# Performance work log

Hardware: AMD Instinct MI355X
Metric: run time of the kernel (lower is better)

## Reference

```python
import jax, jax.numpy as jnp
import numpy as np

B, S, D, H = 2, 2048, 1024, 16
DH = D // H  # 64


def setup_inputs() -> dict:
    key = jax.random.key(0)
    ks = jax.random.split(key, 9)
    def rn(k, shape, scale=1.0):
        return jax.random.normal(k, shape, dtype=jnp.float32) * scale
    w_scale = 1.0 / np.sqrt(D)
    return {
        "queries": rn(ks[0], (B, S, D)),
        "keys": rn(ks[1], (B, S, D)),
        "values": rn(ks[2], (B, S, D)),
        "Wq": rn(ks[3], (D, D), w_scale),
        "bq": rn(ks[4], (D,), w_scale),
        "Wk": rn(ks[5], (D, D), w_scale),
        "bk": rn(ks[6], (D,), w_scale),
        "Wv": rn(ks[7], (D, D), w_scale),
        "bv": rn(ks[8], (D,), w_scale),
    }


def _split_heads(x):
    # torch: cat(split(x, DH, dim=-1), dim=0) -> index (h*B + b); equivalent to
    # [B,S,H,DH] -> [H,B,S,DH]
    bsz, slen, _ = x.shape
    return x.reshape(bsz, slen, H, DH).transpose(2, 0, 1, 3)


def reference(queries, keys, values, Wq, bq, Wk, bk, Wv, bv):
    # Linear projections (W stored so that y = x @ W + b)
    Q = queries @ Wq + bq
    K = keys @ Wk + bk
    V = values @ Wv + bv

    Qh = _split_heads(Q)  # [H,B,S,DH]
    Kh = _split_heads(K)
    Vh = _split_heads(V)

    scale = 1.0 / jnp.sqrt(jnp.asarray(DH, dtype=Qh.dtype))
    scores = jnp.einsum("hbqd,hbkd->hbqk", Qh, Kh) * scale  # [H,B,S,S]
    attn = jax.nn.softmax(scores, axis=-1)  # dropout_rate=0 -> identity
    out = jnp.einsum("hbqk,hbkd->hbqd", attn, Vh)  # [H,B,S,DH]

    # torch: cat(split(out, B, dim=0), dim=2) -> [B,S,H*DH] with head h in slice h
    out = out.transpose(1, 2, 0, 3).reshape(queries.shape[0], queries.shape[1], D)
    return out + queries  # residual; NOTE: W_O is defined but unused in the original forward
```

## Files before the change

kernel.cpp:

```cpp
#include <hip/hip_runtime.h>
#include <hip/hip_bf16.h>
#include <math.h>

#define BB 2
#define SS 2048
#define DD 1024
#define HH 16
#define DHH 64
#define MM (BB * SS)

typedef float f32x4 __attribute__((ext_vector_type(4)));
typedef float f32x16 __attribute__((ext_vector_type(16)));
typedef __bf16 bf16x8 __attribute__((ext_vector_type(8)));
typedef unsigned int u32x2 __attribute__((ext_vector_type(2)));

#define N_QKV ((size_t)MM * DD)
#define N_W   ((size_t)DD * DD)

__device__ unsigned short g_X [3][N_QKV];
__device__ unsigned short g_Q [N_QKV];
__device__ unsigned short g_K [N_QKV];
__device__ unsigned short g_Vt[N_QKV];
__device__ unsigned short g_Wt[3][N_W];

__device__ __forceinline__ unsigned short f2bu(float f) {
    unsigned u = __float_as_uint(f);
    unsigned r = u + 0x7FFFu + ((u >> 16) & 1u);
    return (unsigned short)(r >> 16);
}

union FragU { uint4 u; bf16x8 v; unsigned short s[8]; };
static __device__ __forceinline__ bf16x8 ldfrag(const unsigned short* p) {
    FragU f; f.u = *(const uint4*)p; return f.v;
}

static __device__ __forceinline__ unsigned pkbf(float a, float b) {
    union { __bf16 h[2]; unsigned u; } w;
    w.h[0] = (__bf16)a; w.h[1] = (__bf16)b;
    return w.u;
}

static __device__ __forceinline__ float fexp2(float x) {
#if __has_builtin(__builtin_amdgcn_exp2f)
    return __builtin_amdgcn_exp2f(x);
#else
    float r;
    asm("v_exp_f32 %0, %1" : "=v"(r) : "v"(x));
    return r;
#endif
}

static __device__ __forceinline__ void plswap(unsigned &a, unsigned &b) {
#if __has_builtin(__builtin_amdgcn_permlane32_swap)
    u32x2 r = __builtin_amdgcn_permlane32_swap((int)a, (int)b, false, false);
    a = r[0]; b = r[1];
#else
    asm volatile("v_permlane32_swap_b32 %0, %1" : "+v"(a), "+v"(b));
#endif
}

__global__ __launch_bounds__(256) void cvt3(
        const float* __restrict__ x0, const float* __restrict__ x1,
        const float* __restrict__ x2, unsigned short* __restrict__ X)
{
    const float* src = blockIdx.y == 0 ? x0 : (blockIdx.y == 1 ? x1 : x2);
    unsigned short* dst = X + (size_t)blockIdx.y * N_QKV;
    const size_t i = ((size_t)blockIdx.x * 256 + threadIdx.x) * 4;
    const float4 v = *(const float4*)(src + i);
    ushort4 s;
    s.x = f2bu(v.x); s.y = f2bu(v.y); s.z = f2bu(v.z); s.w = f2bu(v.w);
    *(ushort4*)(dst + i) = s;
}

__global__ __launch_bounds__(256) void transpose_w3(
        const float* __restrict__ W0, const float* __restrict__ W1,
        const float* __restrict__ W2, unsigned short* __restrict__ Wt3)
{
    const float* W = blockIdx.z == 0 ? W0 : (blockIdx.z == 1 ? W1 : W2);
    unsigned short* Wt = Wt3 + (size_t)blockIdx.z * N_W;
    __shared__ float Ts[64][65];
    const int t = threadIdx.x;
    const int k0 = blockIdx.y * 64, n0 = blockIdx.x * 64;
#pragma unroll
    for (int i = 0; i < 16; ++i) {
        const int f = t + 256 * i, r = f >> 6, c = f & 63;
        Ts[r][c] = W[(size_t)(k0 + r) * DD + n0 + c];
    }
    __syncthreads();
#pragma unroll
    for (int i = 0; i < 16; ++i) {
        const int f = t + 256 * i, r = f >> 6, c = f & 63;
        Wt[(size_t)(n0 + r) * DD + k0 + c] = f2bu(Ts[c][r]);
    }
}

__global__ __launch_bounds__(256) void proj3(
        const unsigned short* __restrict__ X, const unsigned short* __restrict__ Wt3,
        const float* __restrict__ bq, const float* __restrict__ bk,
        const float* __restrict__ bv,
        unsigned short* __restrict__ Qp, unsigned short* __restrict__ Kp,
        unsigned short* __restrict__ Vtp)
{
    const int z = blockIdx.z;
    const unsigned short* xb = X   + (size_t)z * N_QKV;
    const unsigned short* Wt = Wt3 + (size_t)z * N_W;
    const float* bias = z == 0 ? bq : (z == 1 ? bk : bv);
    const float scale = z == 0 ? 0.18033688011112042f : 1.0f;

    __shared__ unsigned short As[128][72];
    __shared__ unsigned short Bs[128][72];
    const int t = threadIdx.x, lane = t & 63, w = t >> 6;
    const int q = lane >> 4, li = lane & 15;
    const int wm = (w >> 1) * 64, wn = (w & 1) * 64;
    const int m0 = blockIdx.y * 128, n0 = blockIdx.x * 128;
    const int rs = t >> 3, cs = (t & 7) * 8;

    f32x4 acc[4][4];
#pragma unroll
    for (int mt = 0; mt < 4; ++mt)
#pragma unroll
        for (int nt = 0; nt < 4; ++nt) acc[mt][nt] = (f32x4)0.f;

    uint4 pa0, pa1, pa2, pa3, pb0, pb1, pb2, pb3;
#define PROJ_LD(kk) \
    pa0 = *(const uint4*)(xb + (size_t)(m0 + rs      ) * DD + (kk) + cs); \
    pa1 = *(const uint4*)(xb + (size_t)(m0 + rs + 32 ) * DD + (kk) + cs); \
    pa2 = *(const uint4*)(xb + (size_t)(m0 + rs + 64 ) * DD + (kk) + cs); \
    pa3 = *(const uint4*)(xb + (size_t)(m0 + rs + 96 ) * DD + (kk) + cs); \
    pb0 = *(const uint4*)(Wt + (size_t)(n0 + rs      ) * DD + (kk) + cs); \
    pb1 = *(const uint4*)(Wt + (size_t)(n0 + rs + 32 ) * DD + (kk) + cs); \
    pb2 = *(const uint4*)(Wt + (size_t)(n0 + rs + 64 ) * DD + (kk) + cs); \
    pb3 = *(const uint4*)(Wt + (size_t)(n0 + rs + 96 ) * DD + (kk) + cs);

    PROJ_LD(0)

    for (int kk = 0; kk < DD; kk += 64) {
        *(uint4*)&As[rs     ][cs] = pa0;
        *(uint4*)&As[rs + 32][cs] = pa1;
        *(uint4*)&As[rs + 64][cs] = pa2;
        *(uint4*)&As[rs + 96][cs] = pa3;
        *(uint4*)&Bs[rs     ][cs] = pb0;
        *(uint4*)&Bs[rs + 32][cs] = pb1;
        *(uint4*)&Bs[rs + 64][cs] = pb2;
        *(uint4*)&Bs[rs + 96][cs] = pb3;
        __syncthreads();
        if (kk + 64 < DD) { PROJ_LD(kk + 64) }
#pragma unroll
        for (int ks = 0; ks < 64; ks += 32) {
            bf16x8 a[4], b[4];
#pragma unroll
            for (int mt = 0; mt < 4; ++mt) a[mt] = ldfrag(&As[wm + mt * 16 + li][ks + q * 8]);
#pragma unroll
            for (int nt = 0; nt < 4; ++nt) b[nt] = ldfrag(&Bs[wn + nt * 16 + li][ks + q * 8]);
#pragma unroll
            for (int mt = 0; mt < 4; ++mt)
#pragma unroll
                for (int nt = 0; nt < 4; ++nt)
                    acc[mt][nt] = __builtin_amdgcn_mfma_f32_16x16x32_bf16(
                        a[mt], b[nt], acc[mt][nt], 0, 0, 0);
        }
        __syncthreads();
    }
#undef PROJ_LD

    float bvv[4];
#pragma unroll
    for (int nt = 0; nt < 4; ++nt) bvv[nt] = bias[n0 + wn + nt * 16 + li];

    if (z < 2) {
        unsigned short* out = z == 0 ? Qp : Kp;
#pragma unroll
        for (int mt = 0; mt < 4; ++mt)
#pragma unroll
            for (int nt = 0; nt < 4; ++nt)
#pragma unroll
                for (int reg = 0; reg < 4; ++reg) {
                    const int m = m0 + wm + mt * 16 + q * 4 + reg;
                    out[(size_t)m * DD + n0 + wn + nt * 16 + li] =
                        f2bu((acc[mt][nt][reg] + bvv[nt]) * scale);
                }
    } else {
        const int b = m0 >> 11;
        const int h = (n0 + wn) >> 6;
#pragma unroll
        for (int mt = 0; mt < 4; ++mt)
#pragma unroll
            for (int nt = 0; nt < 4; ++nt) {
                const int s = (m0 & (SS - 1)) + wm + mt * 16 + q * 4;
                const int dh = nt * 16 + li;
                ushort4 sv;
                sv.x = f2bu(acc[mt][nt][0] + bvv[nt]);
                sv.y = f2bu(acc[mt][nt][1] + bvv[nt]);
                sv.z = f2bu(acc[mt][nt][2] + bvv[nt]);
                sv.w = f2bu(acc[mt][nt][3] + bvv[nt]);
                *(ushort4*)(Vtp + ((size_t)((b * HH + h) * DHH + dh)) * SS + s) = sv;
            }
    }
}

__global__ __launch_bounds__(512, 2) void attn9(
        const unsigned short* __restrict__ Qg, const unsigned short* __restrict__ Kg,
        const unsigned short* __restrict__ Vtg,
        const float* __restrict__ queries, float* __restrict__ outp)
{
    __shared__ unsigned short KVb[2][2][2][64][64];
    __shared__ float Lp[2][4][32];

    const int t = threadIdx.x, lane = t & 63;
    const int g  = t >> 8;
    const int wg = (t >> 6) & 3;
    const int col = lane & 31;
    const int hi  = lane >> 5;

    const int bid = blockIdx.x;
    const int slot = bid >> 3;
    const int p = (bid & 7) + 8 * (slot >> 4);
    const int qt = slot & 15;
    const int h = p & 15;
    const int b = p >> 4;

    const int tg = t & 255;
    const int sr = tg >> 3;
    const int sc = tg & 7;

    unsigned short (*Kb)[64][64] = KVb[g][0];
    unsigned short (*Vb)[64][64] = KVb[g][1];

    const unsigned short* Kbase = Kg  + (size_t)(b * SS) * DD + h * DHH;
    const unsigned short* Vbase = Vtg + ((size_t)((b * HH + h) * DHH)) * SS;

    bf16x8 qa[4];
    {
        const unsigned short* qp =
            Qg + (size_t)(b * SS + qt * 128 + wg * 32 + col) * DD + h * DHH + hi * 8;
#pragma unroll
        for (int i = 0; i < 4; ++i) qa[i] = ldfrag(qp + i * 16);
    }

    f32x16 o0 = (f32x16)0.f, o1 = (f32x16)0.f;
    float lsum = 0.f;
    const int xr2 = (col ^ (col >> 3)) & 7;
    const int wsw = (sr ^ (sr >> 3)) & 7;
    const int kvofs = g << 10;

    uint4 aK0, aK1, aV0, aV1, bK0, bK1, bV0, bV1;
#define LD_SET(K0, K1, V0, V1, s0) \
    K0 = *(const uint4*)(Kbase + (size_t)((s0) + sr     ) * DD + sc * 8); \
    K1 = *(const uint4*)(Kbase + (size_t)((s0) + sr + 32) * DD + sc * 8); \
    V0 = *(const uint4*)(Vbase + (size_t)(sr     ) * SS + (s0) + sc * 8); \
    V1 = *(const uint4*)(Vbase + (size_t)(sr + 32) * SS + (s0) + sc * 8);

#define ST_SET(K0, K1, V0, V1, buf) \
    *(uint4*)&Kb[buf][sr     ][(sc ^ wsw) * 8]     = K0; \
    *(uint4*)&Kb[buf][sr + 32][(sc ^ wsw ^ 4) * 8] = K1; \
    *(uint4*)&Vb[buf][sr     ][(sc ^ wsw) * 8]     = V0; \
    *(uint4*)&Vb[buf][sr + 32][(sc ^ wsw ^ 4) * 8] = V1;

#define KT_BODY(CUR, LDG, STG, LDQ4, STQ4)                                    \
    {                                                                         \
        if (LDG) { LD_SET LDQ4 }                                              \
                       \
        f32x16 st0 = (f32x16)0.f, st1 = (f32x16)0.f;                          \
        __builtin_amdgcn_s_setprio(1);                                        \
        _Pragma("unroll")                                                     \
        for (int i = 0; i < 4; ++i) {                                         \
            const int sl = (i * 2 + hi) ^ xr2;                                \
            bf16x8 ka0 = ldfrag(&Kb[CUR][col     ][sl * 8]);                  \
            bf16x8 ka1 = ldfrag(&Kb[CUR][col + 32][(sl ^ 4) * 8]);            \
            st0 = __builtin_amdgcn_mfma_f32_32x32x16_bf16(ka0, qa[i], st0, 0, 0, 0); \
            st1 = __builtin_amdgcn_mfma_f32_32x32x16_bf16(ka1, qa[i], st1, 0, 0, 0); \
        }                                                                     \
        __builtin_amdgcn_s_setprio(0);                                        \
                                 \
        unsigned pkw[4][4];                                                   \
        float ls = 0.f;                                                       \
        _Pragma("unroll")                                                     \
        for (int s = 0; s < 2; ++s) {                                         \
            float pe[8];                                                      \
            _Pragma("unroll")                                                 \
            for (int r = 0; r < 8; ++r) pe[r] = fexp2(st0[8 * s + r]);        \
            ls += ((pe[0] + pe[1]) + (pe[2] + pe[3])) + ((pe[4] + pe[5]) + (pe[6] + pe[7])); \
            pkw[s][0] = pkbf(pe[0], pe[1]); pkw[s][1] = pkbf(pe[2], pe[3]);   \
            pkw[s][2] = pkbf(pe[4], pe[5]); pkw[s][3] = pkbf(pe[6], pe[7]);   \
        }                                                                     \
        _Pragma("unroll")                                                     \
        for (int s = 0; s < 2; ++s) {                                         \
            float pe[8];                                                      \
            _Pragma("unroll")                                                 \
            for (int r = 0; r < 8; ++r) pe[r] = fexp2(st1[8 * s + r]);        \
            ls += ((pe[0] + pe[1]) + (pe[2] + pe[3])) + ((pe[4] + pe[5]) + (pe[6] + pe[7])); \
            pkw[2 + s][0] = pkbf(pe[0], pe[1]); pkw[2 + s][1] = pkbf(pe[2], pe[3]); \
            pkw[2 + s][2] = pkbf(pe[4], pe[5]); pkw[2 + s][3] = pkbf(pe[6], pe[7]); \
        }                                                                     \
        lsum += ls;                                                           \
             \
        if (STG) { ST_SET STQ4 }                                              \
          \
        __builtin_amdgcn_s_setprio(1);                                        \
        _Pragma("unroll")                                                     \
        for (int c = 0; c < 4; ++c) {                                         \
            unsigned A0 = pkw[c][0], B0 = pkw[c][2];                          \
            unsigned A1 = pkw[c][1], B1 = pkw[c][3];                          \
            plswap(A0, B0);                                                   \
            plswap(A1, B1);                                                   \
            FragU pf;                                                         \
            pf.u.x = A0; pf.u.y = A1; pf.u.z = B0; pf.u.w = B1;               \
            const int vl = (c * 2 + hi) ^ xr2;                                \
            bf16x8 vb0 = ldfrag(&Vb[CUR][col     ][vl * 8]);                  \
            bf16x8 vb1 = ldfrag(&Vb[CUR][col + 32][(vl ^ 4) * 8]);            \
            o0 = __builtin_amdgcn_mfma_f32_32x32x16_bf16(pf.v, vb0, o0, 0, 0, 0); \
            o1 = __builtin_amdgcn_mfma_f32_32x32x16_bf16(pf.v, vb1, o1, 0, 0, 0); \
        }                                                                     \
        __builtin_amdgcn_s_setprio(0);                                        \
        __syncthreads();                                                      \
    }

    const int NT = 16;
    LD_SET(aK0, aK1, aV0, aV1, kvofs)
    LD_SET(bK0, bK1, bV0, bV1, kvofs + 64)
    ST_SET(aK0, aK1, aV0, aV1, 0)
    __syncthreads();

    for (int kt = 0; kt < NT; kt += 2) {
        KT_BODY(0, (kt + 2 < NT), (kt + 1 < NT),
                (aK0, aK1, aV0, aV1, kvofs + (kt + 2) * 64),
                (bK0, bK1, bV0, bV1, 1))
        KT_BODY(1, (kt + 3 < NT), (kt + 2 < NT),
                (bK0, bK1, bV0, bV1, kvofs + (kt + 3) * 64),
                (aK0, aK1, aV0, aV1, 0))
    }
#undef KT_BODY
#undef LD_SET
#undef ST_SET

    const float lt = lsum + __shfl_xor(lsum, 32);
    float* Ob = (float*)KVb;
    const int obase = wg * 64 + lane;
    if (g == 1) {
#pragma unroll
        for (int r = 0; r < 16; ++r) {
            Ob[r * 256 + obase]        = o0[r];
            Ob[(16 + r) * 256 + obase] = o1[r];
        }
    }
    if (lane < 32) Lp[g][wg][lane] = lt;
    __syncthreads();

    if (g == 0) {
        const size_t gbase = (size_t)(b * SS + qt * 128 + wg * 32) * DD + h * DHH + col;
#pragma unroll
        for (int reg = 0; reg < 16; ++reg) {
            const int rl = (reg & 3) + 8 * (reg >> 2) + 4 * hi;
            const float li = 1.f / (Lp[0][wg][rl] + Lp[1][wg][rl]);
            const size_t gaddr = gbase + (size_t)rl * DD;
            outp[gaddr]      = (o0[reg] + Ob[reg * 256 + obase]) * li + queries[gaddr];
            outp[gaddr + 32] = (o1[reg] + Ob[(16 + reg) * 256 + obase]) * li + queries[gaddr + 32];
        }
    }
}

extern "C" void kernel_launch(void* const* d_in, const int* in_sizes, int n_in,
                              void* d_out, int out_size, void* d_ws, size_t ws_size,
                              hipStream_t stream) {
    const float* queries = (const float*)d_in[0];
    const float* keys    = (const float*)d_in[1];
    const float* values  = (const float*)d_in[2];
    const float* Wq      = (const float*)d_in[3];
    const float* bq      = (const float*)d_in[4];
    const float* Wk      = (const float*)d_in[5];
    const float* bk      = (const float*)d_in[6];
    const float* Wv      = (const float*)d_in[7];
    const float* bv      = (const float*)d_in[8];
    float* outp = (float*)d_out;

    const size_t need = (6 * N_QKV + 3 * N_W) * sizeof(unsigned short);
    unsigned short *Xp, *Qp, *Kp, *Vtp, *Wtp;
    if (ws_size >= need) {
        Xp  = (unsigned short*)d_ws;
        Qp  = Xp + 3 * N_QKV;
        Kp  = Qp + N_QKV;
        Vtp = Kp + N_QKV;
        Wtp = Vtp + N_QKV;
    } else {
        hipGetSymbolAddress((void**)&Xp,  HIP_SYMBOL(g_X));
        hipGetSymbolAddress((void**)&Qp,  HIP_SYMBOL(g_Q));
        hipGetSymbolAddress((void**)&Kp,  HIP_SYMBOL(g_K));
        hipGetSymbolAddress((void**)&Vtp, HIP_SYMBOL(g_Vt));
        hipGetSymbolAddress((void**)&Wtp, HIP_SYMBOL(g_Wt));
    }

    const dim3 bp(256);
    cvt3<<<dim3(MM * DD / 1024, 3), bp, 0, stream>>>(queries, keys, values, Xp);
    transpose_w3<<<dim3(16, 16, 3), bp, 0, stream>>>(Wq, Wk, Wv, Wtp);
    proj3<<<dim3(8, 32, 3), bp, 0, stream>>>(Xp, Wtp, bq, bk, bv, Qp, Kp, Vtp);
    attn9<<<dim3(512), dim3(512), 0, stream>>>(Qp, Kp, Vtp, queries, outp);
}
```

Baseline: 202.1 us.

## Software-pipeline PV of previous tile with QK of current tile; merge prep kernels

The attention loop is restructured so that the P·V MFMAs for the previous KV tile are interleaved with the Q·K MFMAs of the current tile, using double-buffered probability registers. This lets the exp/softmax work overlap with matrix work and moves the shared-memory store of the next tile after a mid-iteration barrier. Separately, the input conversion and weight transpose kernels are merged into a single launch to remove one launch overhead. It adds register pressure (two pkw arrays plus prefetched fragments), an extra barrier per tile, and a peeled epilogue.

```diff
diff --git a/kernel.cpp b/kernel.cpp
--- a/kernel.cpp
+++ b/kernel.cpp
@@ -59,38 +59,38 @@
 #endif
 }
 
-__global__ __launch_bounds__(256) void cvt3(
+__global__ __launch_bounds__(256) void prep3(
         const float* __restrict__ x0, const float* __restrict__ x1,
-        const float* __restrict__ x2, unsigned short* __restrict__ X)
-{
-    const float* src = blockIdx.y == 0 ? x0 : (blockIdx.y == 1 ? x1 : x2);
-    unsigned short* dst = X + (size_t)blockIdx.y * N_QKV;
-    const size_t i = ((size_t)blockIdx.x * 256 + threadIdx.x) * 4;
-    const float4 v = *(const float4*)(src + i);
-    ushort4 s;
-    s.x = f2bu(v.x); s.y = f2bu(v.y); s.z = f2bu(v.z); s.w = f2bu(v.w);
-    *(ushort4*)(dst + i) = s;
-}
-
-__global__ __launch_bounds__(256) void transpose_w3(
+        const float* __restrict__ x2, unsigned short* __restrict__ X,
         const float* __restrict__ W0, const float* __restrict__ W1,
         const float* __restrict__ W2, unsigned short* __restrict__ Wt3)
 {
-    const float* W = blockIdx.z == 0 ? W0 : (blockIdx.z == 1 ? W1 : W2);
-    unsigned short* Wt = Wt3 + (size_t)blockIdx.z * N_W;
     __shared__ float Ts[64][65];
-    const int t = threadIdx.x;
-    const int k0 = blockIdx.y * 64, n0 = blockIdx.x * 64;
-#pragma unroll
-    for (int i = 0; i < 16; ++i) {
-        const int f = t + 256 * i, r = f >> 6, c = f & 63;
-        Ts[r][c] = W[(size_t)(k0 + r) * DD + n0 + c];
-    }
-    __syncthreads();
-#pragma unroll
-    for (int i = 0; i < 16; ++i) {
-        const int f = t + 256 * i, r = f >> 6, c = f & 63;
-        Wt[(size_t)(n0 + r) * DD + k0 + c] = f2bu(Ts[c][r]);
+    const int z = blockIdx.y, t = threadIdx.x;
+    if (blockIdx.x < 4096) {
+        const float* src = z == 0 ? x0 : (z == 1 ? x1 : x2);
+        unsigned short* dst = X + (size_t)z * N_QKV;
+        const size_t i = ((size_t)blockIdx.x * 256 + t) * 4;
+        const float4 v = *(const float4*)(src + i);
+        ushort4 s;
+        s.x = f2bu(v.x); s.y = f2bu(v.y); s.z = f2bu(v.z); s.w = f2bu(v.w);
+        *(ushort4*)(dst + i) = s;
+    } else {
+        const float* W = z == 0 ? W0 : (z == 1 ? W1 : W2);
+        unsigned short* Wt = Wt3 + (size_t)z * N_W;
+        const int bx = blockIdx.x - 4096;
+        const int k0 = (bx >> 4) * 64, n0 = (bx & 15) * 64;
+#pragma unroll
+        for (int i = 0; i < 16; ++i) {
+            const int f = t + 256 * i, r = f >> 6, c = f & 63;
+            Ts[r][c] = W[(size_t)(k0 + r) * DD + n0 + c];
+        }
+        __syncthreads();
+#pragma unroll
+        for (int i = 0; i < 16; ++i) {
+            const int f = t + 256 * i, r = f >> 6, c = f & 63;
+            Wt[(size_t)(n0 + r) * DD + k0 + c] = f2bu(Ts[c][r]);
+        }
     }
 }
 
@@ -198,7 +198,7 @@
     }
 }
 
-__global__ __launch_bounds__(512, 2) void attn9(
+__global__ __launch_bounds__(512, 2) void attn10(
         const unsigned short* __restrict__ Qg, const unsigned short* __restrict__ Kg,
         const unsigned short* __restrict__ Vtg,
         const float* __restrict__ queries, float* __restrict__ outp)
@@ -244,6 +244,8 @@
     const int kvofs = g << 10;
 
     uint4 aK0, aK1, aV0, aV1, bK0, bK1, bV0, bV1;
+    unsigned pkwE[4][4], pkwO[4][4];
+
 #define LD_SET(K0, K1, V0, V1, s0) \
     K0 = *(const uint4*)(Kbase + (size_t)((s0) + sr     ) * DD + sc * 8); \
     K1 = *(const uint4*)(Kbase + (size_t)((s0) + sr + 32) * DD + sc * 8); \
@@ -256,10 +258,19 @@
     *(uint4*)&Vb[buf][sr     ][(sc ^ wsw) * 8]     = V0; \
     *(uint4*)&Vb[buf][sr + 32][(sc ^ wsw ^ 4) * 8] = V1;
 
-#define KT_BODY(CUR, LDG, STG, LDQ4, STQ4)                                    \
+#define BODY(CUR, PKW_C, PKW_P, DO_PREV, LDG, LDQ, STG, STQ)                  \
     {                                                                         \
-        if (LDG) { LD_SET LDQ4 }                                              \
-                       \
+        if (LDG) { LD_SET LDQ }                                               \
+        FragU pf[4];                                                          \
+        if (DO_PREV) {                                                        \
+            _Pragma("unroll")                                                 \
+            for (int c = 0; c < 4; ++c) {                                     \
+                unsigned A0 = PKW_P[c][0], B0 = PKW_P[c][2];                  \
+                unsigned A1 = PKW_P[c][1], B1 = PKW_P[c][3];                  \
+                plswap(A0, B0); plswap(A1, B1);                               \
+                pf[c].u.x = A0; pf[c].u.y = A1; pf[c].u.z = B0; pf[c].u.w = B1; \
+            }                                                                 \
+        }                                                                     \
         f32x16 st0 = (f32x16)0.f, st1 = (f32x16)0.f;                          \
         __builtin_amdgcn_s_setprio(1);                                        \
         _Pragma("unroll")                                                     \
@@ -269,10 +280,17 @@
             bf16x8 ka1 = ldfrag(&Kb[CUR][col + 32][(sl ^ 4) * 8]);            \
             st0 = __builtin_amdgcn_mfma_f32_32x32x16_bf16(ka0, qa[i], st0, 0, 0, 0); \
             st1 = __builtin_amdgcn_mfma_f32_32x32x16_bf16(ka1, qa[i], st1, 0, 0, 0); \
+            if (DO_PREV) {                                                    \
+                bf16x8 vb0 = ldfrag(&Vb[(CUR) ^ 1][col     ][sl * 8]);        \
+                bf16x8 vb1 = ldfrag(&Vb[(CUR) ^ 1][col + 32][(sl ^ 4) * 8]);  \
+                o0 = __builtin_amdgcn_mfma_f32_32x32x16_bf16(pf[i].v, vb0, o0, 0, 0, 0); \
+                o1 = __builtin_amdgcn_mfma_f32_32x32x16_bf16(pf[i].v, vb1, o1, 0, 0, 0); \
+            }                                                                 \
         }                                                                     \
         __builtin_amdgcn_s_setprio(0);                                        \
-                                 \
-        unsigned pkw[4][4];                                                   \
+        __syncthreads();                 \
+        if (STG) { ST_SET STQ }        \
+                    \
         float ls = 0.f;                                                       \
         _Pragma("unroll")                                                     \
         for (int s = 0; s < 2; ++s) {                                         \
@@ -280,8 +298,8 @@
             _Pragma("unroll")                                                 \
             for (int r = 0; r < 8; ++r) pe[r] = fexp2(st0[8 * s + r]);        \
             ls += ((pe[0] + pe[1]) + (pe[2] + pe[3])) + ((pe[4] + pe[5]) + (pe[6] + pe[7])); \
-            pkw[s][0] = pkbf(pe[0], pe[1]); pkw[s][1] = pkbf(pe[2], pe[3]);   \
-            pkw[s][2] = pkbf(pe[4], pe[5]); pkw[s][3] = pkbf(pe[6], pe[7]);   \
+            PKW_C[s][0] = pkbf(pe[0], pe[1]); PKW_C[s][1] = pkbf(pe[2], pe[3]); \
+            PKW_C[s][2] = pkbf(pe[4], pe[5]); PKW_C[s][3] = pkbf(pe[6], pe[7]); \
         }                                                                     \
         _Pragma("unroll")                                                     \
         for (int s = 0; s < 2; ++s) {                                         \
@@ -289,30 +307,11 @@
             _Pragma("unroll")                                                 \
             for (int r = 0; r < 8; ++r) pe[r] = fexp2(st1[8 * s + r]);        \
             ls += ((pe[0] + pe[1]) + (pe[2] + pe[3])) + ((pe[4] + pe[5]) + (pe[6] + pe[7])); \
-            pkw[2 + s][0] = pkbf(pe[0], pe[1]); pkw[2 + s][1] = pkbf(pe[2], pe[3]); \
-            pkw[2 + s][2] = pkbf(pe[4], pe[5]); pkw[2 + s][3] = pkbf(pe[6], pe[7]); \
+            PKW_C[2 + s][0] = pkbf(pe[0], pe[1]); PKW_C[2 + s][1] = pkbf(pe[2], pe[3]); \
+            PKW_C[2 + s][2] = pkbf(pe[4], pe[5]); PKW_C[2 + s][3] = pkbf(pe[6], pe[7]); \
         }                                                                     \
         lsum += ls;                                                           \
-             \
-        if (STG) { ST_SET STQ4 }                                              \
-          \
-        __builtin_amdgcn_s_setprio(1);                                        \
-        _Pragma("unroll")                                                     \
-        for (int c = 0; c < 4; ++c) {                                         \
-            unsigned A0 = pkw[c][0], B0 = pkw[c][2];                          \
-            unsigned A1 = pkw[c][1], B1 = pkw[c][3];                          \
-            plswap(A0, B0);                                                   \
-            plswap(A1, B1);                                                   \
-            FragU pf;                                                         \
-            pf.u.x = A0; pf.u.y = A1; pf.u.z = B0; pf.u.w = B1;               \
-            const int vl = (c * 2 + hi) ^ xr2;                                \
-            bf16x8 vb0 = ldfrag(&Vb[CUR][col     ][vl * 8]);                  \
-            bf16x8 vb1 = ldfrag(&Vb[CUR][col + 32][(vl ^ 4) * 8]);            \
-            o0 = __builtin_amdgcn_mfma_f32_32x32x16_bf16(pf.v, vb0, o0, 0, 0, 0); \
-            o1 = __builtin_amdgcn_mfma_f32_32x32x16_bf16(pf.v, vb1, o1, 0, 0, 0); \
-        }                                                                     \
-        __builtin_amdgcn_s_setprio(0);                                        \
-        __syncthreads();                                                      \
+        __syncthreads();                      \
     }
 
     const int NT = 16;
@@ -321,15 +320,36 @@
     ST_SET(aK0, aK1, aV0, aV1, 0)
     __syncthreads();
 
-    for (int kt = 0; kt < NT; kt += 2) {
-        KT_BODY(0, (kt + 2 < NT), (kt + 1 < NT),
-                (aK0, aK1, aV0, aV1, kvofs + (kt + 2) * 64),
-                (bK0, bK1, bV0, bV1, 1))
-        KT_BODY(1, (kt + 3 < NT), (kt + 2 < NT),
-                (bK0, bK1, bV0, bV1, kvofs + (kt + 3) * 64),
-                (aK0, aK1, aV0, aV1, 0))
-    }
-#undef KT_BODY
+    BODY(0, pkwE, pkwO, false, true, (aK0, aK1, aV0, aV1, kvofs + 128),
+         true, (bK0, bK1, bV0, bV1, 1))
+
+    for (int kt = 1; kt <= 13; kt += 2) {
+        BODY(1, pkwO, pkwE, true, true, (bK0, bK1, bV0, bV1, kvofs + (kt + 2) * 64),
+             true, (aK0, aK1, aV0, aV1, 0))
+        BODY(0, pkwE, pkwO, true, (kt + 3 < NT),
+             (aK0, aK1, aV0, aV1, kvofs + (kt + 3) * 64),
+             true, (bK0, bK1, bV0, bV1, 1))
+    }
+    BODY(1, pkwO, pkwE, true, false, (bK0, bK1, bV0, bV1, 0),
+         false, (aK0, aK1, aV0, aV1, 0))
+
+    {
+#pragma unroll
+        for (int c = 0; c < 4; ++c) {
+            unsigned A0 = pkwO[c][0], B0 = pkwO[c][2];
+            unsigned A1 = pkwO[c][1], B1 = pkwO[c][3];
+            plswap(A0, B0); plswap(A1, B1);
+            FragU pf;
+            pf.u.x = A0; pf.u.y = A1; pf.u.z = B0; pf.u.w = B1;
+            const int sl = (c * 2 + hi) ^ xr2;
+            bf16x8 vb0 = ldfrag(&Vb[1][col     ][sl * 8]);
+            bf16x8 vb1 = ldfrag(&Vb[1][col + 32][(sl ^ 4) * 8]);
+            o0 = __builtin_amdgcn_mfma_f32_32x32x16_bf16(pf.v, vb0, o0, 0, 0, 0);
+            o1 = __builtin_amdgcn_mfma_f32_32x32x16_bf16(pf.v, vb1, o1, 0, 0, 0);
+        }
+    }
+    __syncthreads();
+#undef BODY
 #undef LD_SET
 #undef ST_SET
 
@@ -390,8 +410,8 @@
     }
 
     const dim3 bp(256);
-    cvt3<<<dim3(MM * DD / 1024, 3), bp, 0, stream>>>(queries, keys, values, Xp);
-    transpose_w3<<<dim3(16, 16, 3), bp, 0, stream>>>(Wq, Wk, Wv, Wtp);
+    prep3<<<dim3(4096 + 256, 3), bp, 0, stream>>>(queries, keys, values, Xp,
+                                                  Wq, Wk, Wv, Wtp);
     proj3<<<dim3(8, 32, 3), bp, 0, stream>>>(Xp, Wtp, bq, bk, bv, Qp, Kp, Vtp);
-    attn9<<<dim3(512), dim3(512), 0, stream>>>(Qp, Kp, Vtp, queries, outp);
-}
+    attn10<<<dim3(512), dim3(512), 0, stream>>>(Qp, Kp, Vtp, queries, outp);
+}
```

Result: no change. 200.4 us (-0.9%).

## Restructure attention to 256-row query tiles, fuse prep kernels, remap projection blocks

Applied to the files above, without the earlier changes.

The attention kernel drops the split-KV scheme, where two 256-thread groups each covered half the keys and merged partial results through LDS. Now each 512-thread block covers 256 query rows with 8 waves over the full key range. K/V tiles go through a 4-buffer LDS pipeline that loads two 64-key tiles per step, and barriers happen every two tiles instead of every tile. The bf16 conversion and weight transpose kernels are merged into one launch, and projection blocks are launched on a 1D grid with a swizzled block-to-tile mapping. In exchange, attention runs only 256 blocks at one block per CU, which lowers occupancy and removes the extra parallelism the key split provided.

```diff
diff --git a/kernel.cpp b/kernel.cpp
--- a/kernel.cpp
+++ b/kernel.cpp
@@ -59,38 +59,38 @@
 #endif
 }
 
-__global__ __launch_bounds__(256) void cvt3(
+__global__ __launch_bounds__(256) void prep3(
         const float* __restrict__ x0, const float* __restrict__ x1,
-        const float* __restrict__ x2, unsigned short* __restrict__ X)
-{
-    const float* src = blockIdx.y == 0 ? x0 : (blockIdx.y == 1 ? x1 : x2);
-    unsigned short* dst = X + (size_t)blockIdx.y * N_QKV;
-    const size_t i = ((size_t)blockIdx.x * 256 + threadIdx.x) * 4;
-    const float4 v = *(const float4*)(src + i);
-    ushort4 s;
-    s.x = f2bu(v.x); s.y = f2bu(v.y); s.z = f2bu(v.z); s.w = f2bu(v.w);
-    *(ushort4*)(dst + i) = s;
-}
-
-__global__ __launch_bounds__(256) void transpose_w3(
+        const float* __restrict__ x2, unsigned short* __restrict__ X,
         const float* __restrict__ W0, const float* __restrict__ W1,
         const float* __restrict__ W2, unsigned short* __restrict__ Wt3)
 {
-    const float* W = blockIdx.z == 0 ? W0 : (blockIdx.z == 1 ? W1 : W2);
-    unsigned short* Wt = Wt3 + (size_t)blockIdx.z * N_W;
     __shared__ float Ts[64][65];
-    const int t = threadIdx.x;
-    const int k0 = blockIdx.y * 64, n0 = blockIdx.x * 64;
-#pragma unroll
-    for (int i = 0; i < 16; ++i) {
-        const int f = t + 256 * i, r = f >> 6, c = f & 63;
-        Ts[r][c] = W[(size_t)(k0 + r) * DD + n0 + c];
-    }
-    __syncthreads();
-#pragma unroll
-    for (int i = 0; i < 16; ++i) {
-        const int f = t + 256 * i, r = f >> 6, c = f & 63;
-        Wt[(size_t)(n0 + r) * DD + k0 + c] = f2bu(Ts[c][r]);
+    const int z = blockIdx.y, t = threadIdx.x;
+    if (blockIdx.x < 4096) {
+        const float* src = z == 0 ? x0 : (z == 1 ? x1 : x2);
+        unsigned short* dst = X + (size_t)z * N_QKV;
+        const size_t i = ((size_t)blockIdx.x * 256 + t) * 4;
+        const float4 v = *(const float4*)(src + i);
+        ushort4 s;
+        s.x = f2bu(v.x); s.y = f2bu(v.y); s.z = f2bu(v.z); s.w = f2bu(v.w);
+        *(ushort4*)(dst + i) = s;
+    } else {
+        const float* W = z == 0 ? W0 : (z == 1 ? W1 : W2);
+        unsigned short* Wt = Wt3 + (size_t)z * N_W;
+        const int bx = blockIdx.x - 4096;
+        const int k0 = (bx >> 4) * 64, n0 = (bx & 15) * 64;
+#pragma unroll
+        for (int i = 0; i < 16; ++i) {
+            const int f = t + 256 * i, r = f >> 6, c = f & 63;
+            Ts[r][c] = W[(size_t)(k0 + r) * DD + n0 + c];
+        }
+        __syncthreads();
+#pragma unroll
+        for (int i = 0; i < 16; ++i) {
+            const int f = t + 256 * i, r = f >> 6, c = f & 63;
+            Wt[(size_t)(n0 + r) * DD + k0 + c] = f2bu(Ts[c][r]);
+        }
     }
 }
 
@@ -101,7 +101,13 @@
         unsigned short* __restrict__ Qp, unsigned short* __restrict__ Kp,
         unsigned short* __restrict__ Vtp)
 {
-    const int z = blockIdx.z;
+    const int bid = blockIdx.x;
+    const int xx = bid & 7, j = bid >> 3;
+    const int zm = xx * 12 + (j >> 3);
+    const int z  = zm >> 5;
+    const int m0 = (zm & 31) * 128;
+    const int n0 = (j & 7) * 128;
+
     const unsigned short* xb = X   + (size_t)z * N_QKV;
     const unsigned short* Wt = Wt3 + (size_t)z * N_W;
     const float* bias = z == 0 ? bq : (z == 1 ? bk : bv);
@@ -112,7 +118,6 @@
     const int t = threadIdx.x, lane = t & 63, w = t >> 6;
     const int q = lane >> 4, li = lane & 15;
     const int wm = (w >> 1) * 64, wn = (w & 1) * 64;
-    const int m0 = blockIdx.y * 128, n0 = blockIdx.x * 128;
     const int rs = t >> 3, cs = (t & 7) * 8;
 
     f32x4 acc[4][4];
@@ -198,33 +203,26 @@
     }
 }
 
-__global__ __launch_bounds__(512, 2) void attn9(
+__global__ __launch_bounds__(512, 1) void attn11(
         const unsigned short* __restrict__ Qg, const unsigned short* __restrict__ Kg,
         const unsigned short* __restrict__ Vtg,
         const float* __restrict__ queries, float* __restrict__ outp)
 {
-    __shared__ unsigned short KVb[2][2][2][64][64];
-    __shared__ float Lp[2][4][32];
-
-    const int t = threadIdx.x, lane = t & 63;
-    const int g  = t >> 8;
-    const int wg = (t >> 6) & 3;
+    __shared__ unsigned short Kb[4][64][64];
+    __shared__ unsigned short Vb[4][64][64];
+    __shared__ float Lp[8][32];
+
+    const int t = threadIdx.x, lane = t & 63, w = t >> 6;
     const int col = lane & 31;
     const int hi  = lane >> 5;
 
     const int bid = blockIdx.x;
-    const int slot = bid >> 3;
-    const int p = (bid & 7) + 8 * (slot >> 4);
-    const int qt = slot & 15;
-    const int h = p & 15;
-    const int b = p >> 4;
-
-    const int tg = t & 255;
-    const int sr = tg >> 3;
-    const int sc = tg & 7;
-
-    unsigned short (*Kb)[64][64] = KVb[g][0];
-    unsigned short (*Vb)[64][64] = KVb[g][1];
+    const int p  = (bid & 7) * 4 + ((bid >> 3) >> 3);
+    const int qt = (bid >> 3) & 7;
+    const int h = p & 15, b = p >> 4;
+
+    const int sr = t >> 3;
+    const int sc = t & 7;
 
     const unsigned short* Kbase = Kg  + (size_t)(b * SS) * DD + h * DHH;
     const unsigned short* Vbase = Vtg + ((size_t)((b * HH + h) * DHH)) * SS;
@@ -232,7 +230,7 @@
     bf16x8 qa[4];
     {
         const unsigned short* qp =
-            Qg + (size_t)(b * SS + qt * 128 + wg * 32 + col) * DD + h * DHH + hi * 8;
+            Qg + (size_t)(b * SS + qt * 256 + w * 32 + col) * DD + h * DHH + hi * 8;
 #pragma unroll
         for (int i = 0; i < 4; ++i) qa[i] = ldfrag(qp + i * 16);
     }
@@ -241,37 +239,33 @@
     float lsum = 0.f;
     const int xr2 = (col ^ (col >> 3)) & 7;
     const int wsw = (sr ^ (sr >> 3)) & 7;
-    const int kvofs = g << 10;
-
-    uint4 aK0, aK1, aV0, aV1, bK0, bK1, bV0, bV1;
-#define LD_SET(K0, K1, V0, V1, s0) \
-    K0 = *(const uint4*)(Kbase + (size_t)((s0) + sr     ) * DD + sc * 8); \
-    K1 = *(const uint4*)(Kbase + (size_t)((s0) + sr + 32) * DD + sc * 8); \
-    V0 = *(const uint4*)(Vbase + (size_t)(sr     ) * SS + (s0) + sc * 8); \
-    V1 = *(const uint4*)(Vbase + (size_t)(sr + 32) * SS + (s0) + sc * 8);
-
-#define ST_SET(K0, K1, V0, V1, buf) \
-    *(uint4*)&Kb[buf][sr     ][(sc ^ wsw) * 8]     = K0; \
-    *(uint4*)&Kb[buf][sr + 32][(sc ^ wsw ^ 4) * 8] = K1; \
-    *(uint4*)&Vb[buf][sr     ][(sc ^ wsw) * 8]     = V0; \
-    *(uint4*)&Vb[buf][sr + 32][(sc ^ wsw ^ 4) * 8] = V1;
-
-#define KT_BODY(CUR, LDG, STG, LDQ4, STQ4)                                    \
+
+    uint4 aK0, aV0, aK1, aV1, bK0, bV0, bK1, bV1;
+#define LD2(K0, V0, K1, V1, s0) \
+    K0 = *(const uint4*)(Kbase + (size_t)((s0)      + sr) * DD + sc * 8); \
+    V0 = *(const uint4*)(Vbase + (size_t)sr * SS + (s0)      + sc * 8); \
+    K1 = *(const uint4*)(Kbase + (size_t)((s0) + 64 + sr) * DD + sc * 8); \
+    V1 = *(const uint4*)(Vbase + (size_t)sr * SS + (s0) + 64 + sc * 8);
+
+#define ST2(K0, V0, K1, V1, b0, b1) \
+    *(uint4*)&Kb[b0][sr][(sc ^ wsw) * 8] = K0; \
+    *(uint4*)&Vb[b0][sr][(sc ^ wsw) * 8] = V0; \
+    *(uint4*)&Kb[b1][sr][(sc ^ wsw) * 8] = K1; \
+    *(uint4*)&Vb[b1][sr][(sc ^ wsw) * 8] = V1;
+
+#define TILE(BUF)                                                             \
     {                                                                         \
-        if (LDG) { LD_SET LDQ4 }                                              \
-                       \
         f32x16 st0 = (f32x16)0.f, st1 = (f32x16)0.f;                          \
         __builtin_amdgcn_s_setprio(1);                                        \
         _Pragma("unroll")                                                     \
         for (int i = 0; i < 4; ++i) {                                         \
             const int sl = (i * 2 + hi) ^ xr2;                                \
-            bf16x8 ka0 = ldfrag(&Kb[CUR][col     ][sl * 8]);                  \
-            bf16x8 ka1 = ldfrag(&Kb[CUR][col + 32][(sl ^ 4) * 8]);            \
+            bf16x8 ka0 = ldfrag(&Kb[BUF][col     ][sl * 8]);                  \
+            bf16x8 ka1 = ldfrag(&Kb[BUF][col + 32][(sl ^ 4) * 8]);            \
             st0 = __builtin_amdgcn_mfma_f32_32x32x16_bf16(ka0, qa[i], st0, 0, 0, 0); \
             st1 = __builtin_amdgcn_mfma_f32_32x32x16_bf16(ka1, qa[i], st1, 0, 0, 0); \
         }                                                                     \
         __builtin_amdgcn_s_setprio(0);                                        \
-                                 \
         unsigned pkw[4][4];                                                   \
         float ls = 0.f;                                                       \
         _Pragma("unroll")                                                     \
@@ -293,69 +287,56 @@
             pkw[2 + s][2] = pkbf(pe[4], pe[5]); pkw[2 + s][3] = pkbf(pe[6], pe[7]); \
         }                                                                     \
         lsum += ls;                                                           \
-             \
-        if (STG) { ST_SET STQ4 }                                              \
-          \
         __builtin_amdgcn_s_setprio(1);                                        \
         _Pragma("unroll")                                                     \
         for (int c = 0; c < 4; ++c) {                                         \
             unsigned A0 = pkw[c][0], B0 = pkw[c][2];                          \
             unsigned A1 = pkw[c][1], B1 = pkw[c][3];                          \
-            plswap(A0, B0);                                                   \
-            plswap(A1, B1);                                                   \
+            plswap(A0, B0); plswap(A1, B1);                                   \
             FragU pf;                                                         \
             pf.u.x = A0; pf.u.y = A1; pf.u.z = B0; pf.u.w = B1;               \
             const int vl = (c * 2 + hi) ^ xr2;                                \
-            bf16x8 vb0 = ldfrag(&Vb[CUR][col     ][vl * 8]);                  \
-            bf16x8 vb1 = ldfrag(&Vb[CUR][col + 32][(vl ^ 4) * 8]);            \
+            bf16x8 vb0 = ldfrag(&Vb[BUF][col     ][vl * 8]);                  \
+            bf16x8 vb1 = ldfrag(&Vb[BUF][col + 32][(vl ^ 4) * 8]);            \
             o0 = __builtin_amdgcn_mfma_f32_32x32x16_bf16(pf.v, vb0, o0, 0, 0, 0); \
             o1 = __builtin_amdgcn_mfma_f32_32x32x16_bf16(pf.v, vb1, o1, 0, 0, 0); \
         }                                                                     \
         __builtin_amdgcn_s_setprio(0);                                        \
-        __syncthreads();                                                      \
-    }
-
-    const int NT = 16;
-    LD_SET(aK0, aK1, aV0, aV1, kvofs)
-    LD_SET(bK0, bK1, bV0, bV1, kvofs + 64)
-    ST_SET(aK0, aK1, aV0, aV1, 0)
+    }
+
+    LD2(aK0, aV0, aK1, aV1, 0)
+    ST2(aK0, aV0, aK1, aV1, 0, 1)
+    LD2(bK0, bV0, bK1, bV1, 128)
     __syncthreads();
 
-    for (int kt = 0; kt < NT; kt += 2) {
-        KT_BODY(0, (kt + 2 < NT), (kt + 1 < NT),
-                (aK0, aK1, aV0, aV1, kvofs + (kt + 2) * 64),
-                (bK0, bK1, bV0, bV1, 1))
-        KT_BODY(1, (kt + 3 < NT), (kt + 2 < NT),
-                (bK0, bK1, bV0, bV1, kvofs + (kt + 3) * 64),
-                (aK0, aK1, aV0, aV1, 0))
-    }
-#undef KT_BODY
-#undef LD_SET
-#undef ST_SET
+    for (int tt = 0; tt < SS; tt += 256) {
+        if (tt + 256 < SS) { LD2(aK0, aV0, aK1, aV1, tt + 256) }
+        TILE(0)
+        ST2(bK0, bV0, bK1, bV1, 2, 3)
+        TILE(1)
+        __syncthreads();
+        if (tt + 384 < SS) { LD2(bK0, bV0, bK1, bV1, tt + 384) }
+        TILE(2)
+        if (tt + 256 < SS) { ST2(aK0, aV0, aK1, aV1, 0, 1) }
+        TILE(3)
+        if (tt + 256 < SS) __syncthreads();
+    }
+#undef TILE
+#undef LD2
+#undef ST2
 
     const float lt = lsum + __shfl_xor(lsum, 32);
-    float* Ob = (float*)KVb;
-    const int obase = wg * 64 + lane;
-    if (g == 1) {
-#pragma unroll
-        for (int r = 0; r < 16; ++r) {
-            Ob[r * 256 + obase]        = o0[r];
-            Ob[(16 + r) * 256 + obase] = o1[r];
-        }
-    }
-    if (lane < 32) Lp[g][wg][lane] = lt;
+    if (lane < 32) Lp[w][lane] = lt;
     __syncthreads();
 
-    if (g == 0) {
-        const size_t gbase = (size_t)(b * SS + qt * 128 + wg * 32) * DD + h * DHH + col;
-#pragma unroll
-        for (int reg = 0; reg < 16; ++reg) {
-            const int rl = (reg & 3) + 8 * (reg >> 2) + 4 * hi;
-            const float li = 1.f / (Lp[0][wg][rl] + Lp[1][wg][rl]);
-            const size_t gaddr = gbase + (size_t)rl * DD;
-            outp[gaddr]      = (o0[reg] + Ob[reg * 256 + obase]) * li + queries[gaddr];
-            outp[gaddr + 32] = (o1[reg] + Ob[(16 + reg) * 256 + obase]) * li + queries[gaddr + 32];
-        }
+    const size_t gbase = (size_t)(b * SS + qt * 256 + w * 32) * DD + h * DHH + col;
+#pragma unroll
+    for (int reg = 0; reg < 16; ++reg) {
+        const int rl = (reg & 3) + 8 * (reg >> 2) + 4 * hi;
+        const float li = 1.f / Lp[w][rl];
+        const size_t g = gbase + (size_t)rl * DD;
+        outp[g]      = o0[reg] * li + queries[g];
+        outp[g + 32] = o1[reg] * li + queries[g + 32];
     }
 }
 
@@ -390,8 +371,8 @@
     }
 
     const dim3 bp(256);
-    cvt3<<<dim3(MM * DD / 1024, 3), bp, 0, stream>>>(queries, keys, values, Xp);
-    transpose_w3<<<dim3(16, 16, 3), bp, 0, stream>>>(Wq, Wk, Wv, Wtp);
-    proj3<<<dim3(8, 32, 3), bp, 0, stream>>>(Xp, Wtp, bq, bk, bv, Qp, Kp, Vtp);
-    attn9<<<dim3(512), dim3(512), 0, stream>>>(Qp, Kp, Vtp, queries, outp);
-}
+    prep3<<<dim3(4096 + 256, 3), bp, 0, stream>>>(queries, keys, values, Xp,
+                                                  Wq, Wk, Wv, Wtp);
+    proj3<<<dim3(768), bp, 0, stream>>>(Xp, Wtp, bq, bk, bv, Qp, Kp, Vtp);
+    attn11<<<dim3(256), dim3(512), 0, stream>>>(Qp, Kp, Vtp, queries, outp);
+}
```

After: 193.5 us. 4.3% less time.
